# Optimization experiments

Hardware: AMD Instinct MI355X
Metric: run time of the kernel (lower is better)

## Reference

```python
import jax, jax.numpy as jnp
import numpy as np

NUM_FIELDS = 39
VOCAB_PER_FIELD = 1000
EMB = 64
HEADS = 2
LAYERS = 3
BATCH = 16384
FLAT = NUM_FIELDS * EMB  # 2496


def _mhsa(x, Wq, Wk, Wv, Wr):
    # x: [B, n, D]; no scaling (scaling=False in source)
    B, n, D = x.shape
    dh = D // HEADS
    q = (x @ Wq).reshape(B, n, HEADS, dh)
    k = (x @ Wk).reshape(B, n, HEADS, dh)
    v = (x @ Wv).reshape(B, n, HEADS, dh)
    scores = jnp.einsum('bihd,bjhd->bhij', q, k)
    attn = jax.nn.softmax(scores, axis=-1)
    out = jnp.einsum('bhij,bjhd->bihd', attn, v).reshape(B, n, D)
    out = out + x @ Wr  # residual projection (use_res=True)
    return jax.nn.relu(out)


def setup_inputs() -> dict:
    key = jax.random.key(0)
    ks = jax.random.split(key, 12)
    X = jax.random.randint(ks[0], (BATCH, NUM_FIELDS), 0, VOCAB_PER_FIELD, dtype=jnp.int64 if jax.config.jax_enable_x64 else jnp.int32)
    emb_table = jax.random.normal(ks[1], (NUM_FIELDS * VOCAB_PER_FIELD, EMB), jnp.float32) * 0.05
    WQ = jax.random.normal(ks[2], (LAYERS, EMB, EMB), jnp.float32) * 0.05
    WK = jax.random.normal(ks[3], (LAYERS, EMB, EMB), jnp.float32) * 0.05
    WV = jax.random.normal(ks[4], (LAYERS, EMB, EMB), jnp.float32) * 0.05
    WR = jax.random.normal(ks[5], (LAYERS, EMB, EMB), jnp.float32) * 0.05
    W1 = jax.random.normal(ks[6], (FLAT, 512), jnp.float32) * 0.02
    b1 = jnp.zeros((512,), jnp.float32)
    W2 = jax.random.normal(ks[7], (512, 256), jnp.float32) * 0.02
    b2 = jnp.zeros((256,), jnp.float32)
    W3 = jax.random.normal(ks[8], (256, 1), jnp.float32) * 0.02
    b3 = jnp.zeros((1,), jnp.float32)
    Wlin = jax.random.normal(ks[9], (FLAT, 1), jnp.float32) * 0.02
    return {"X": X, "emb_table": emb_table, "WQ": WQ, "WK": WK, "WV": WV,
            "WR": WR, "W1": W1, "b1": b1, "W2": W2, "b2": b2, "W3": W3,
            "b3": b3, "Wlin": Wlin}


def reference(X, emb_table, WQ, WK, WV, WR, W1, b1, W2, b2, W3, b3, Wlin):
    offsets = jnp.arange(NUM_FIELDS, dtype=X.dtype) * VOCAB_PER_FIELD
    embed_x = emb_table[X + offsets[None, :]]  # [B, n, D]
    att = embed_x
    for i in range(LAYERS):
        att = _mhsa(att, WQ[i], WK[i], WV[i], WR[i])
    B = att.shape[0]
    att_output = jax.nn.relu(att.reshape(B, FLAT) @ Wlin)  # [B,1]
    # MLP: relu follows every Dense, including final 1-unit layer; dropout inactive
    h = embed_x.reshape(B, FLAT)
    h = jax.nn.relu(h @ W1 + b1)
    h = jax.nn.relu(h @ W2 + b2)
    dnn_output = jax.nn.relu(h @ W3 + b3)  # [B,1]
    return jax.nn.sigmoid(att_output + dnn_output)
```

## Files before the change

kernel.cpp:

```cpp
#include <hip/hip_runtime.h>
#include <hip/hip_bf16.h>


#define NF     39
#define EMB    64
#define NLAYER 3
#define VOCAB  1000
#define FLAT   2496
#define H1     512
#define H2     256

typedef __attribute__((ext_vector_type(8))) short  short8;
typedef __attribute__((ext_vector_type(4))) float  floatx4;

__device__ __forceinline__ short8 ld8s(const unsigned short* p) {
    return *(const short8*)p;
}
__device__ __forceinline__ float b2f(unsigned short h) {
    union { unsigned u; float f; } x; x.u = ((unsigned)h) << 16; return x.f;
}
__device__ __forceinline__ unsigned short f2b(float f) {
    union { float f; unsigned u; } x; x.f = f;
    unsigned u = x.u;
    return (unsigned short)((u + 0x7fffu + ((u >> 16) & 1u)) >> 16);
}
__device__ __forceinline__ unsigned cvt_pk(float a, float b) {
#if defined(__gfx950__)
    unsigned r;
    asm("v_cvt_pk_bf16_f32 %0, %1, %2" : "=v"(r) : "v"(a), "v"(b));
    return r;
#else
    return (unsigned)f2b(a) | ((unsigned)f2b(b) << 16);
#endif
}

__global__ void attw_t(const float* __restrict__ WQ, const float* __restrict__ WK,
                       const float* __restrict__ WV, const float* __restrict__ WR,
                       unsigned short* __restrict__ wqt, unsigned short* __restrict__ wkt,
                       unsigned short* __restrict__ wvt, unsigned short* __restrict__ wrt)
{
    int idx = blockIdx.x * 256 + threadIdx.x;
    if (idx >= 4 * 3 * 4096) return;
    int mat = idx / 12288;
    int rem = idx % 12288;
    int l   = rem / 4096;
    int ok  = rem % 4096;
    int o = ok >> 6, k = ok & 63;
    const float*    src = (mat == 0) ? WQ : (mat == 1) ? WK : (mat == 2) ? WV : WR;
    unsigned short* dst = (mat == 0) ? wqt : (mat == 1) ? wkt : (mat == 2) ? wvt : wrt;
    dst[l * 4096 + o * 64 + k] = f2b(src[l * 4096 + k * 64 + o]);
}

__global__ void w1pack(const float* __restrict__ W1, unsigned short* __restrict__ w1p)
{
    int t = blockIdx.x * 256 + threadIdx.x;
    int lane = t & 63, grp = t >> 6;
    int ot = grp / 78, kk = grp % 78;
    int q = lane >> 4, n = ot * 16 + (lane & 15);
    int kb = kk * 32 + q * 8;
    unsigned short* dst = w1p + grp * 512 + lane * 8;
    #pragma unroll
    for (int j = 0; j < 8; ++j)
        dst[j] = f2b(W1[(kb + j) * 512 + n]);
}

__global__ void w2pack(const float* __restrict__ W2, unsigned short* __restrict__ w2p)
{
    int t = blockIdx.x * 256 + threadIdx.x;
    int lane = t & 63, grp = t >> 6;
    int ot = grp / 16, kk = grp % 16;
    int q = lane >> 4, n = ot * 16 + (lane & 15);
    int kb = kk * 32 + q * 8;
    unsigned short* dst = w2p + grp * 512 + lane * 8;
    #pragma unroll
    for (int j = 0; j < 8; ++j)
        dst[j] = f2b(W2[(kb + j) * 256 + n]);
}

__global__ void __launch_bounds__(128) attn_kernel(
    const int* __restrict__ X,
    const float* __restrict__ embf,
    const unsigned short* __restrict__ wqt,
    const unsigned short* __restrict__ wkt,
    const unsigned short* __restrict__ wvt,
    const unsigned short* __restrict__ wrt,
    const float* __restrict__ wlinf,
    float* __restrict__ att_out)
{
    __shared__ unsigned short xss[48 * 72];
    __shared__ unsigned short arena[2][4736];
    __shared__ float red[2];

    const int tid  = threadIdx.x;
    const int wid  = tid >> 6;
    const int lane = tid & 63;
    const int h    = wid;
    const int quad = lane >> 4;
    const int l16  = lane & 15;
    const int samp = blockIdx.x;

    unsigned short* qs  = arena[wid];
    unsigned short* ks  = qs + 1920;
    unsigned short* Ps  = qs;
    unsigned short* vt  = qs + 3456;

    {
        const int tq = lane >> 4;
        const int cp = (lane & 15) * 2;
        const int col = h * 32 + cp;
        const int* xrow = X + samp * NF;
        #pragma unroll
        for (int t0 = 0; t0 < 48; t0 += 4) {
            int t = t0 + tq;
            unsigned pk = 0;
            if (t < NF) {
                int row = xrow[t] + t * VOCAB;
                const float2 v = *(const float2*)&embf[row * EMB + col];
                pk = cvt_pk(v.x, v.y);
            }
            *(unsigned*)&xss[t * 72 + col] = pk;
        }
    }
    __syncthreads();

    for (int layer = 0; layer < NLAYER; ++layer) {
        const unsigned short* wq  = wqt + layer * 4096;
        const unsigned short* wk  = wkt + layer * 4096;
        const unsigned short* wvp = wvt + layer * 4096;
        const unsigned short* wr  = wrt + layer * 4096;

        #pragma unroll
        for (int mat = 0; mat < 2; ++mat) {
            const unsigned short* wt = mat ? wk : wq;
            unsigned short* dst = mat ? ks : qs;
            #pragma unroll
            for (int ot = 0; ot < 2; ++ot) {
                #pragma unroll
                for (int tt = 0; tt < 3; ++tt) {
                    floatx4 c = {0.f, 0.f, 0.f, 0.f};
                    #pragma unroll
                    for (int kk = 0; kk < 2; ++kk) {
                        short8 a = ld8s(&wt[(h * 32 + ot * 16 + l16) * 64 + kk * 32 + quad * 8]);
                        short8 b = ld8s(&xss[(tt * 16 + l16) * 72 + kk * 32 + quad * 8]);
                        c = __builtin_amdgcn_mfma_f32_16x16x32_bf16(a, b, c, 0, 0, 0);
                    }
                    uint2 w;
                    w.x = cvt_pk(c[0], c[1]);
                    w.y = cvt_pk(c[2], c[3]);
                    *(uint2*)&dst[(tt * 16 + l16) * 40 + ot * 16 + quad * 4] = w;
                }
            }
        }

        floatx4 O[2][3];
        #pragma unroll
        for (int dt = 0; dt < 2; ++dt) {
            #pragma unroll
            for (int it = 0; it < 3; ++it) {
                floatx4 c = {0.f, 0.f, 0.f, 0.f};
                #pragma unroll
                for (int kk = 0; kk < 2; ++kk) {
                    short8 a = ld8s(&wr[(h * 32 + dt * 16 + l16) * 64 + kk * 32 + quad * 8]);
                    short8 b = ld8s(&xss[(it * 16 + l16) * 72 + kk * 32 + quad * 8]);
                    c = __builtin_amdgcn_mfma_f32_16x16x32_bf16(a, b, c, 0, 0, 0);
                }
                O[dt][it] = c;
            }
        }

        floatx4 ST[3][3];
        #pragma unroll
        for (int jt = 0; jt < 3; ++jt) {
            short8 a = ld8s(&ks[(jt * 16 + l16) * 40 + quad * 8]);
            #pragma unroll
            for (int it = 0; it < 3; ++it) {
                short8 b = ld8s(&qs[(it * 16 + l16) * 40 + quad * 8]);
                floatx4 z = {0.f, 0.f, 0.f, 0.f};
                ST[jt][it] = __builtin_amdgcn_mfma_f32_16x16x32_bf16(a, b, z, 0, 0, 0);
            }
        }

        #pragma unroll
        for (int it = 0; it < 3; ++it) {
            float p[3][4];
            float sum = 0.f;
            #pragma unroll
            for (int jt = 0; jt < 3; ++jt)
                #pragma unroll
                for (int r = 0; r < 4; ++r) {
                    int j = jt * 16 + quad * 4 + r;
                    float e = (j < NF) ? __expf(ST[jt][it][r]) : 0.f;
                    p[jt][r] = e;
                    sum += e;
                }
            sum += __shfl_xor(sum, 16, 64);
            sum += __shfl_xor(sum, 32, 64);
            float inv = 1.0f / sum;
            #pragma unroll
            for (int jt = 0; jt < 3; ++jt) {
                uint2 w;
                w.x = cvt_pk(p[jt][0] * inv, p[jt][1] * inv);
                w.y = cvt_pk(p[jt][2] * inv, p[jt][3] * inv);
                *(uint2*)&Ps[(it * 16 + l16) * 72 + jt * 16 + quad * 4] = w;
            }
            uint2 z2; z2.x = 0; z2.y = 0;
            *(uint2*)&Ps[(it * 16 + l16) * 72 + 48 + quad * 4] = z2;
        }

        unsigned sv[2][2];
        #pragma unroll
        for (int mt = 0; mt < 3; ++mt) {
            #pragma unroll
            for (int nt = 0; nt < 2; ++nt) {
                floatx4 c = {0.f, 0.f, 0.f, 0.f};
                #pragma unroll
                for (int kk = 0; kk < 2; ++kk) {
                    short8 a = ld8s(&xss[(mt * 16 + l16) * 72 + kk * 32 + quad * 8]);
                    short8 b = ld8s(&wvp[(h * 32 + nt * 16 + l16) * 64 + kk * 32 + quad * 8]);
                    c = __builtin_amdgcn_mfma_f32_16x16x32_bf16(a, b, c, 0, 0, 0);
                }
                unsigned lo = cvt_pk(c[0], c[1]);
                unsigned hi = cvt_pk(c[2], c[3]);
                if (mt < 2) {
                    uint2 w; w.x = lo; w.y = hi;
                    *(uint2*)&vt[(nt * 16 + l16) * 40 + mt * 16 + quad * 4] = w;
                } else {
                    sv[nt][0] = lo; sv[nt][1] = hi;
                }
            }
        }

        {
            short8 b0 = ld8s(&Ps[(l16) * 72 + quad * 8]);
            short8 b1 = ld8s(&Ps[(16 + l16) * 72 + quad * 8]);
            short8 b2 = ld8s(&Ps[(32 + l16) * 72 + quad * 8]);
            #pragma unroll
            for (int dt = 0; dt < 2; ++dt) {
                short8 a = ld8s(&vt[(dt * 16 + l16) * 40 + quad * 8]);
                O[dt][0] = __builtin_amdgcn_mfma_f32_16x16x32_bf16(a, b0, O[dt][0], 0, 0, 0);
                O[dt][1] = __builtin_amdgcn_mfma_f32_16x16x32_bf16(a, b1, O[dt][1], 0, 0, 0);
                O[dt][2] = __builtin_amdgcn_mfma_f32_16x16x32_bf16(a, b2, O[dt][2], 0, 0, 0);
            }
        }
        #pragma unroll
        for (int nt = 0; nt < 2; ++nt) {
            uint2 w; w.x = sv[nt][0]; w.y = sv[nt][1];
            *(uint2*)&vt[(nt * 16 + l16) * 40 + quad * 4] = w;
            uint2 z; z.x = 0; z.y = 0;
            *(uint2*)&vt[(nt * 16 + l16) * 40 + 16 + quad * 4] = z;
        }
        {
            short8 b0 = ld8s(&Ps[(l16) * 72 + 32 + quad * 8]);
            short8 b1 = ld8s(&Ps[(16 + l16) * 72 + 32 + quad * 8]);
            short8 b2 = ld8s(&Ps[(32 + l16) * 72 + 32 + quad * 8]);
            #pragma unroll
            for (int dt = 0; dt < 2; ++dt) {
                short8 a = ld8s(&vt[(dt * 16 + l16) * 40 + quad * 8]);
                O[dt][0] = __builtin_amdgcn_mfma_f32_16x16x32_bf16(a, b0, O[dt][0], 0, 0, 0);
                O[dt][1] = __builtin_amdgcn_mfma_f32_16x16x32_bf16(a, b1, O[dt][1], 0, 0, 0);
                O[dt][2] = __builtin_amdgcn_mfma_f32_16x16x32_bf16(a, b2, O[dt][2], 0, 0, 0);
            }
        }

        __syncthreads();

        #pragma unroll
        for (int dt = 0; dt < 2; ++dt)
            #pragma unroll
            for (int it = 0; it < 3; ++it) {
                uint2 w;
                w.x = cvt_pk(fmaxf(O[dt][it][0], 0.f), fmaxf(O[dt][it][1], 0.f));
                w.y = cvt_pk(fmaxf(O[dt][it][2], 0.f), fmaxf(O[dt][it][3], 0.f));
                *(uint2*)&xss[(it * 16 + l16) * 72 + h * 32 + dt * 16 + quad * 4] = w;
            }

        __syncthreads();
    }

    {
        float acc = 0.f;
        const int c = lane & 31, tp = lane >> 5;
        const int col = h * 32 + c;
        for (int t0 = 0; t0 < 40; t0 += 2) {
            int t = t0 + tp;
            if (t < NF)
                acc += b2f(xss[t * 72 + col]) * wlinf[t * EMB + col];
        }
        #pragma unroll
        for (int off = 1; off < 64; off <<= 1)
            acc += __shfl_xor(acc, off, 64);
        if (lane == 0) red[wid] = acc;
        __syncthreads();
        if (tid == 0)
            att_out[samp] = fmaxf(red[0] + red[1], 0.f);
    }
}

__global__ void __launch_bounds__(256) dnn_kernel(
    const int* __restrict__ X,
    const float* __restrict__ embf,
    const unsigned short* __restrict__ w1p,
    const float* __restrict__ b1v,
    const unsigned short* __restrict__ w2p,
    const float* __restrict__ b2v,
    const float* __restrict__ w3v,
    const float* __restrict__ b3v,
    const float* __restrict__ att_in,
    float* __restrict__ out)
{
    __shared__ unsigned short ea[2][32 * 72];
    __shared__ unsigned short h1s[32 * 520];
    unsigned short* h2s = h1s;

    const int tid  = threadIdx.x;
    const int wid  = tid >> 6, lane = tid & 63, quad = lane >> 4, l16 = lane & 15;
    const int S0   = blockIdx.x * 32;

    floatx4 C1[2][8];
    #pragma unroll
    for (int mt = 0; mt < 2; ++mt)
        #pragma unroll
        for (int nt = 0; nt < 8; ++nt)
            C1[mt][nt] = (floatx4){0.f, 0.f, 0.f, 0.f};

    const int gs = tid >> 3;
    const int gg = tid & 7;

    {
        int row = X[(S0 + gs) * NF + 0];
        const float4* src = (const float4*)&embf[row * EMB + gg * 8];
        float4 v0 = src[0], v1 = src[1];
        uint4 u;
        u.x = cvt_pk(v0.x, v0.y); u.y = cvt_pk(v0.z, v0.w);
        u.z = cvt_pk(v1.x, v1.y); u.w = cvt_pk(v1.z, v1.w);
        *(uint4*)&ea[0][gs * 72 + gg * 8] = u;
    }
    __syncthreads();

    for (int f = 0; f < NF; ++f) {
        if (f < NF - 1) {
            int row = X[(S0 + gs) * NF + f + 1] + (f + 1) * VOCAB;
            const float4* src = (const float4*)&embf[row * EMB + gg * 8];
            float4 v0 = src[0], v1 = src[1];
            uint4 u;
            u.x = cvt_pk(v0.x, v0.y); u.y = cvt_pk(v0.z, v0.w);
            u.z = cvt_pk(v1.x, v1.y); u.w = cvt_pk(v1.z, v1.w);
            *(uint4*)&ea[(f + 1) & 1][gs * 72 + gg * 8] = u;
        }
        const unsigned short* eac = ea[f & 1];
        short8 a[2][2];
        #pragma unroll
        for (int mt = 0; mt < 2; ++mt) {
            a[mt][0] = ld8s(&eac[(mt * 16 + l16) * 72 + quad * 8]);
            a[mt][1] = ld8s(&eac[(mt * 16 + l16) * 72 + 32 + quad * 8]);
        }
        #pragma unroll
        for (int nt = 0; nt < 8; ++nt) {
            const unsigned short* bp = w1p + (((wid * 8 + nt) * 78 + f * 2) * 64 + lane) * 8;
            short8 b0 = ld8s(bp);
            short8 b1 = ld8s(bp + 512);
            #pragma unroll
            for (int mt = 0; mt < 2; ++mt) {
                C1[mt][nt] = __builtin_amdgcn_mfma_f32_16x16x32_bf16(a[mt][0], b0, C1[mt][nt], 0, 0, 0);
                C1[mt][nt] = __builtin_amdgcn_mfma_f32_16x16x32_bf16(a[mt][1], b1, C1[mt][nt], 0, 0, 0);
            }
        }
        __syncthreads();
    }

    #pragma unroll
    for (int nt = 0; nt < 8; ++nt) {
        float bb = b1v[wid * 128 + nt * 16 + l16];
        #pragma unroll
        for (int mt = 0; mt < 2; ++mt) {
            #pragma unroll
            for (int r = 0; r < 4; ++r) {
                float v = fmaxf(C1[mt][nt][r] + bb, 0.f);
                h1s[(mt * 16 + quad * 4 + r) * 520 + wid * 128 + nt * 16 + l16] = f2b(v);
            }
        }
    }
    __syncthreads();

    floatx4 C2[2][4];
    #pragma unroll
    for (int mt = 0; mt < 2; ++mt)
        #pragma unroll
        for (int nt = 0; nt < 4; ++nt)
            C2[mt][nt] = (floatx4){0.f, 0.f, 0.f, 0.f};

    #pragma unroll 4
    for (int kk = 0; kk < 16; ++kk) {
        short8 a0 = ld8s(&h1s[(l16) * 520 + kk * 32 + quad * 8]);
        short8 a1 = ld8s(&h1s[(16 + l16) * 520 + kk * 32 + quad * 8]);
        #pragma unroll
        for (int nt = 0; nt < 4; ++nt) {
            short8 b = ld8s(w2p + (((wid * 4 + nt) * 16 + kk) * 64 + lane) * 8);
            C2[0][nt] = __builtin_amdgcn_mfma_f32_16x16x32_bf16(a0, b, C2[0][nt], 0, 0, 0);
            C2[1][nt] = __builtin_amdgcn_mfma_f32_16x16x32_bf16(a1, b, C2[1][nt], 0, 0, 0);
        }
    }
    __syncthreads();

    #pragma unroll
    for (int nt = 0; nt < 4; ++nt) {
        float bb = b2v[wid * 64 + nt * 16 + l16];
        #pragma unroll
        for (int mt = 0; mt < 2; ++mt)
            #pragma unroll
            for (int r = 0; r < 4; ++r)
                h2s[(mt * 16 + quad * 4 + r) * 264 + wid * 64 + nt * 16 + l16] =
                    f2b(fmaxf(C2[mt][nt][r] + bb, 0.f));
    }
    __syncthreads();

    {
        int s = tid >> 3, part = tid & 7;
        float acc = 0.f;
        #pragma unroll 8
        for (int j = 0; j < 32; ++j) {
            int jj = part * 32 + j;
            acc += b2f(h2s[s * 264 + jj]) * w3v[jj];
        }
        acc += __shfl_xor(acc, 1, 64);
        acc += __shfl_xor(acc, 2, 64);
        acc += __shfl_xor(acc, 4, 64);
        if (part == 0) {
            float dnn = fmaxf(acc + b3v[0], 0.f);
            float v = dnn + att_in[S0 + s];
            out[S0 + s] = 1.f / (1.f + __expf(-v));
        }
    }
}

extern "C" void kernel_launch(void* const* d_in, const int* in_sizes, int n_in,
                              void* d_out, int out_size, void* d_ws, size_t ws_size,
                              hipStream_t stream)
{
    (void)in_sizes; (void)n_in; (void)out_size; (void)ws_size;

    const int*   X    = (const int*)d_in[0];
    const float* emb  = (const float*)d_in[1];
    const float* WQ   = (const float*)d_in[2];
    const float* WK   = (const float*)d_in[3];
    const float* WV   = (const float*)d_in[4];
    const float* WR   = (const float*)d_in[5];
    const float* W1   = (const float*)d_in[6];
    const float* b1   = (const float*)d_in[7];
    const float* W2   = (const float*)d_in[8];
    const float* b2   = (const float*)d_in[9];
    const float* W3   = (const float*)d_in[10];
    const float* b3   = (const float*)d_in[11];
    const float* Wlin = (const float*)d_in[12];

    char* ws = (char*)d_ws;
    float*          att_logit = (float*)ws;
    unsigned short* wqt = (unsigned short*)(ws + 65536);
    unsigned short* wkt = wqt + 3 * 4096;
    unsigned short* wvt = wkt + 3 * 4096;
    unsigned short* wrt = wvt + 3 * 4096;
    unsigned short* w1p = wrt + 3 * 4096;
    unsigned short* w2p = w1p + 2496 * 512;

    attw_t<<<192, 256, 0, stream>>>(WQ, WK, WV, WR, wqt, wkt, wvt, wrt);
    w1pack<<<624, 256, 0, stream>>>(W1, w1p);
    w2pack<<<64, 256, 0, stream>>>(W2, w2p);
    attn_kernel<<<16384, 128, 0, stream>>>(X, emb, wqt, wkt, wvt, wrt, Wlin, att_logit);
    dnn_kernel<<<512, 256, 0, stream>>>(X, emb, w1p, b1, w2p, b2, W3, b3, att_logit,
                                        (float*)d_out);
}
```

Measured before the change: 401.7 us.

## Keep Q, K, V and softmax probabilities in registers instead of LDS

The per-layer attention now loads the input tile from shared memory once into register fragments and reuses them for the Q, K, V and residual MFMAs. MFMA output fragments are repacked directly as bf16 operands for the QK^T and PV MFMAs. This relies on both operands using the same permuted K-index order, which removes the per-wave LDS arena and its store/load round trips. The cost is higher register pressure, plus a barrier that now sits after the input fragment load.

```diff
diff --git a/kernel.cpp b/kernel.cpp
--- a/kernel.cpp
+++ b/kernel.cpp
@@ -32,6 +32,11 @@
 #else
     return (unsigned)f2b(a) | ((unsigned)f2b(b) << 16);
 #endif
+}
+__device__ __forceinline__ short8 pk8(unsigned a, unsigned b, unsigned c, unsigned d) {
+    union { unsigned u[4]; short8 s; } x;
+    x.u[0] = a; x.u[1] = b; x.u[2] = c; x.u[3] = d;
+    return x.s;
 }
 
 __global__ void attw_t(const float* __restrict__ WQ, const float* __restrict__ WK,
@@ -88,7 +93,6 @@
     float* __restrict__ att_out)
 {
     __shared__ unsigned short xss[48 * 72];
-    __shared__ unsigned short arena[2][4736];
     __shared__ float red[2];
 
     const int tid  = threadIdx.x;
@@ -99,11 +103,6 @@
     const int l16  = lane & 15;
     const int samp = blockIdx.x;
 
-    unsigned short* qs  = arena[wid];
-    unsigned short* ks  = qs + 1920;
-    unsigned short* Ps  = qs;
-    unsigned short* vt  = qs + 3456;
-
     {
         const int tq = lane >> 4;
         const int cp = (lane & 15) * 2;
@@ -129,25 +128,35 @@
         const unsigned short* wvp = wvt + layer * 4096;
         const unsigned short* wr  = wrt + layer * 4096;
 
+        short8 xf[3][2];
+        #pragma unroll
+        for (int tt = 0; tt < 3; ++tt)
+            #pragma unroll
+            for (int kk = 0; kk < 2; ++kk)
+                xf[tt][kk] = ld8s(&xss[(tt * 16 + l16) * 72 + kk * 32 + quad * 8]);
+
+        __syncthreads();
+
+        unsigned qw[2][3][2], kw[2][3][2];
         #pragma unroll
         for (int mat = 0; mat < 2; ++mat) {
             const unsigned short* wt = mat ? wk : wq;
-            unsigned short* dst = mat ? ks : qs;
             #pragma unroll
             for (int ot = 0; ot < 2; ++ot) {
+                short8 w0 = ld8s(&wt[(h * 32 + ot * 16 + l16) * 64 + quad * 8]);
+                short8 w1 = ld8s(&wt[(h * 32 + ot * 16 + l16) * 64 + 32 + quad * 8]);
                 #pragma unroll
                 for (int tt = 0; tt < 3; ++tt) {
                     floatx4 c = {0.f, 0.f, 0.f, 0.f};
-                    #pragma unroll
-                    for (int kk = 0; kk < 2; ++kk) {
-                        short8 a = ld8s(&wt[(h * 32 + ot * 16 + l16) * 64 + kk * 32 + quad * 8]);
-                        short8 b = ld8s(&xss[(tt * 16 + l16) * 72 + kk * 32 + quad * 8]);
-                        c = __builtin_amdgcn_mfma_f32_16x16x32_bf16(a, b, c, 0, 0, 0);
+                    c = __builtin_amdgcn_mfma_f32_16x16x32_bf16(w0, xf[tt][0], c, 0, 0, 0);
+                    c = __builtin_amdgcn_mfma_f32_16x16x32_bf16(w1, xf[tt][1], c, 0, 0, 0);
+                    if (mat == 0) {
+                        qw[ot][tt][0] = cvt_pk(c[0], c[1]);
+                        qw[ot][tt][1] = cvt_pk(c[2], c[3]);
+                    } else {
+                        kw[ot][tt][0] = cvt_pk(c[0], c[1]);
+                        kw[ot][tt][1] = cvt_pk(c[2], c[3]);
                     }
-                    uint2 w;
-                    w.x = cvt_pk(c[0], c[1]);
-                    w.y = cvt_pk(c[2], c[3]);
-                    *(uint2*)&dst[(tt * 16 + l16) * 40 + ot * 16 + quad * 4] = w;
                 }
             }
         }
@@ -155,15 +164,13 @@
         floatx4 O[2][3];
         #pragma unroll
         for (int dt = 0; dt < 2; ++dt) {
+            short8 w0 = ld8s(&wr[(h * 32 + dt * 16 + l16) * 64 + quad * 8]);
+            short8 w1 = ld8s(&wr[(h * 32 + dt * 16 + l16) * 64 + 32 + quad * 8]);
             #pragma unroll
             for (int it = 0; it < 3; ++it) {
                 floatx4 c = {0.f, 0.f, 0.f, 0.f};
-                #pragma unroll
-                for (int kk = 0; kk < 2; ++kk) {
-                    short8 a = ld8s(&wr[(h * 32 + dt * 16 + l16) * 64 + kk * 32 + quad * 8]);
-                    short8 b = ld8s(&xss[(it * 16 + l16) * 72 + kk * 32 + quad * 8]);
-                    c = __builtin_amdgcn_mfma_f32_16x16x32_bf16(a, b, c, 0, 0, 0);
-                }
+                c = __builtin_amdgcn_mfma_f32_16x16x32_bf16(w0, xf[it][0], c, 0, 0, 0);
+                c = __builtin_amdgcn_mfma_f32_16x16x32_bf16(w1, xf[it][1], c, 0, 0, 0);
                 O[dt][it] = c;
             }
         }
@@ -171,15 +178,31 @@
         floatx4 ST[3][3];
         #pragma unroll
         for (int jt = 0; jt < 3; ++jt) {
-            short8 a = ld8s(&ks[(jt * 16 + l16) * 40 + quad * 8]);
+            short8 a = pk8(kw[0][jt][0], kw[0][jt][1], kw[1][jt][0], kw[1][jt][1]);
             #pragma unroll
             for (int it = 0; it < 3; ++it) {
-                short8 b = ld8s(&qs[(it * 16 + l16) * 40 + quad * 8]);
+                short8 b = pk8(qw[0][it][0], qw[0][it][1], qw[1][it][0], qw[1][it][1]);
                 floatx4 z = {0.f, 0.f, 0.f, 0.f};
                 ST[jt][it] = __builtin_amdgcn_mfma_f32_16x16x32_bf16(a, b, z, 0, 0, 0);
             }
         }
 
+        unsigned vw[3][2][2];
+        #pragma unroll
+        for (int nt = 0; nt < 2; ++nt) {
+            short8 w0 = ld8s(&wvp[(h * 32 + nt * 16 + l16) * 64 + quad * 8]);
+            short8 w1 = ld8s(&wvp[(h * 32 + nt * 16 + l16) * 64 + 32 + quad * 8]);
+            #pragma unroll
+            for (int mt = 0; mt < 3; ++mt) {
+                floatx4 c = {0.f, 0.f, 0.f, 0.f};
+                c = __builtin_amdgcn_mfma_f32_16x16x32_bf16(xf[mt][0], w0, c, 0, 0, 0);
+                c = __builtin_amdgcn_mfma_f32_16x16x32_bf16(xf[mt][1], w1, c, 0, 0, 0);
+                vw[mt][nt][0] = cvt_pk(c[0], c[1]);
+                vw[mt][nt][1] = cvt_pk(c[2], c[3]);
+            }
+        }
+
+        unsigned pw[3][3][2];
         #pragma unroll
         for (int it = 0; it < 3; ++it) {
             float p[3][4];
@@ -198,71 +221,23 @@
             float inv = 1.0f / sum;
             #pragma unroll
             for (int jt = 0; jt < 3; ++jt) {
-                uint2 w;
-                w.x = cvt_pk(p[jt][0] * inv, p[jt][1] * inv);
-                w.y = cvt_pk(p[jt][2] * inv, p[jt][3] * inv);
-                *(uint2*)&Ps[(it * 16 + l16) * 72 + jt * 16 + quad * 4] = w;
-            }
-            uint2 z2; z2.x = 0; z2.y = 0;
-            *(uint2*)&Ps[(it * 16 + l16) * 72 + 48 + quad * 4] = z2;
-        }
-
-        unsigned sv[2][2];
-        #pragma unroll
-        for (int mt = 0; mt < 3; ++mt) {
-            #pragma unroll
-            for (int nt = 0; nt < 2; ++nt) {
-                floatx4 c = {0.f, 0.f, 0.f, 0.f};
-                #pragma unroll
-                for (int kk = 0; kk < 2; ++kk) {
-                    short8 a = ld8s(&xss[(mt * 16 + l16) * 72 + kk * 32 + quad * 8]);
-                    short8 b = ld8s(&wvp[(h * 32 + nt * 16 + l16) * 64 + kk * 32 + quad * 8]);
-                    c = __builtin_amdgcn_mfma_f32_16x16x32_bf16(a, b, c, 0, 0, 0);
-                }
-                unsigned lo = cvt_pk(c[0], c[1]);
-                unsigned hi = cvt_pk(c[2], c[3]);
-                if (mt < 2) {
-                    uint2 w; w.x = lo; w.y = hi;
-                    *(uint2*)&vt[(nt * 16 + l16) * 40 + mt * 16 + quad * 4] = w;
-                } else {
-                    sv[nt][0] = lo; sv[nt][1] = hi;
-                }
-            }
-        }
-
-        {
-            short8 b0 = ld8s(&Ps[(l16) * 72 + quad * 8]);
-            short8 b1 = ld8s(&Ps[(16 + l16) * 72 + quad * 8]);
-            short8 b2 = ld8s(&Ps[(32 + l16) * 72 + quad * 8]);
-            #pragma unroll
-            for (int dt = 0; dt < 2; ++dt) {
-                short8 a = ld8s(&vt[(dt * 16 + l16) * 40 + quad * 8]);
-                O[dt][0] = __builtin_amdgcn_mfma_f32_16x16x32_bf16(a, b0, O[dt][0], 0, 0, 0);
-                O[dt][1] = __builtin_amdgcn_mfma_f32_16x16x32_bf16(a, b1, O[dt][1], 0, 0, 0);
-                O[dt][2] = __builtin_amdgcn_mfma_f32_16x16x32_bf16(a, b2, O[dt][2], 0, 0, 0);
-            }
-        }
-        #pragma unroll
-        for (int nt = 0; nt < 2; ++nt) {
-            uint2 w; w.x = sv[nt][0]; w.y = sv[nt][1];
-            *(uint2*)&vt[(nt * 16 + l16) * 40 + quad * 4] = w;
-            uint2 z; z.x = 0; z.y = 0;
-            *(uint2*)&vt[(nt * 16 + l16) * 40 + 16 + quad * 4] = z;
-        }
-        {
-            short8 b0 = ld8s(&Ps[(l16) * 72 + 32 + quad * 8]);
-            short8 b1 = ld8s(&Ps[(16 + l16) * 72 + 32 + quad * 8]);
-            short8 b2 = ld8s(&Ps[(32 + l16) * 72 + 32 + quad * 8]);
-            #pragma unroll
-            for (int dt = 0; dt < 2; ++dt) {
-                short8 a = ld8s(&vt[(dt * 16 + l16) * 40 + quad * 8]);
-                O[dt][0] = __builtin_amdgcn_mfma_f32_16x16x32_bf16(a, b0, O[dt][0], 0, 0, 0);
-                O[dt][1] = __builtin_amdgcn_mfma_f32_16x16x32_bf16(a, b1, O[dt][1], 0, 0, 0);
-                O[dt][2] = __builtin_amdgcn_mfma_f32_16x16x32_bf16(a, b2, O[dt][2], 0, 0, 0);
-            }
-        }
-
-        __syncthreads();
+                pw[jt][it][0] = cvt_pk(p[jt][0] * inv, p[jt][1] * inv);
+                pw[jt][it][1] = cvt_pk(p[jt][2] * inv, p[jt][3] * inv);
+            }
+        }
+
+        #pragma unroll
+        for (int dt = 0; dt < 2; ++dt) {
+            short8 a01 = pk8(vw[0][dt][0], vw[0][dt][1], vw[1][dt][0], vw[1][dt][1]);
+            short8 a2  = pk8(vw[2][dt][0], vw[2][dt][1], 0u, 0u);
+            #pragma unroll
+            for (int it = 0; it < 3; ++it) {
+                short8 b01 = pk8(pw[0][it][0], pw[0][it][1], pw[1][it][0], pw[1][it][1]);
+                short8 b2  = pk8(pw[2][it][0], pw[2][it][1], 0u, 0u);
+                O[dt][it] = __builtin_amdgcn_mfma_f32_16x16x32_bf16(a01, b01, O[dt][it], 0, 0, 0);
+                O[dt][it] = __builtin_amdgcn_mfma_f32_16x16x32_bf16(a2,  b2,  O[dt][it], 0, 0, 0);
+            }
+        }
 
         #pragma unroll
         for (int dt = 0; dt < 2; ++dt)
```

New measurement: 382.5 us, median of 2. 4.8% less time.
